# Performance work log

Measured on AMD Instinct MI355X. Metric: run time of the kernel, lower is better.

## Reference

```python
import jax, jax.numpy as jnp
import numpy as np

B, L, D, N_HEADS = 4, 8192, 1024, 16
HD = D // N_HEADS
MASK_NEG = -1e10


def setup_inputs() -> dict:
    key = jax.random.key(0)
    ks = jax.random.split(key, 5)
    # xavier_normal std for square Dense: sqrt(2/(fan_in+fan_out))
    std = (2.0 / (D + D)) ** 0.5
    return {
        "query": jax.random.normal(ks[0], (B, L, D), dtype=jnp.float32),
        "mask": jax.random.bernoulli(ks[1], 0.1, (B, L)),  # True = masked out
        "Wq": std * jax.random.normal(ks[2], (D, D), dtype=jnp.float32),
        "bq": jnp.zeros((D,), dtype=jnp.float32),
        "Wk": std * jax.random.normal(ks[3], (D, D), dtype=jnp.float32),
        "bk": jnp.zeros((D,), dtype=jnp.float32),
        "Wv": std * jax.random.normal(ks[4], (D, D), dtype=jnp.float32),
        "bv": jnp.zeros((D,), dtype=jnp.float32),
    }


def reference(query, mask, Wq, bq, Wk, bk, Wv, bv):
    # Self-attention: key = value = query (original falls back when key/value are None)
    q = query @ Wq + bq  # [B, L, D]
    k = query @ Wk + bk
    v = query @ Wv + bv
    # split heads: b l (n h) -> b l n h
    qs = q.reshape(B, L, N_HEADS, HD)
    ks_ = k.reshape(B, L, N_HEADS, HD)
    vs = v.reshape(B, L, N_HEADS, HD)
    m = mask[:, :, None, None]  # [B, L, 1, 1], broadcast over heads & dims
    K = jnp.where(m, MASK_NEG, ks_)
    V = jnp.where(m, 0.0, vs)
    # elu kernel feature map: phi(x) = elu(x) + 1 (elu(-1e10)+1 -> 0 for masked keys)
    phiK = jax.nn.elu(K) + 1.0
    phiQ = jax.nn.elu(qs) + 1.0
    # per-head kv summary: [B, N, HD_k, HD_v]
    kv = jnp.einsum('blnk,blnv->bnkv', phiK, V)
    # FAITHFUL to original einsum 'blk,bkv->blk': sums kv over v, elementwise with phiQ
    kv_sum = kv.sum(-1)  # [B, N, HD]
    out = phiQ * kv_sum[:, None, :, :]  # [B, L, N, HD]
    # combine heads: b l n h -> b l (n h)
    return out.reshape(B, L, D)
```

## Files before the change

### kernel.cpp

```cpp
#include <hip/hip_runtime.h>

typedef unsigned short u16;
typedef unsigned int u32;
typedef __attribute__((ext_vector_type(8))) short s16x8;
typedef __attribute__((ext_vector_type(4))) float f32x4;

#define GAS __attribute__((address_space(1)))
#define LAS __attribute__((address_space(3)))

#define BB 4
#define LL 8192
#define DD 1024
#define NH 16
#define HD 64
#define MROWS (BB * LL)
#define NWBT 2064

__device__ __forceinline__ u16 f2bf(float f) {
  u32 u = __builtin_bit_cast(u32, f);
  u32 r = (u + 0x7FFFu + ((u >> 16) & 1u)) >> 16;
  return (u16)r;
}
__device__ __forceinline__ float bf2f(u32 lo) {
  return __builtin_bit_cast(float, lo << 16);
}

__device__ __forceinline__ void async16(const void* g, void* l) {
  __builtin_amdgcn_global_load_lds((const GAS u32*)g, (LAS u32*)l, 16, 0, 0);
}

__device__ __forceinline__ bool get_mask(const void* mp, int row, int mode) {
  if (mode == 2) return ((const unsigned char*)mp)[row] != 0;
  if (mode == 1) return ((const float*)mp)[row] != 0.f;
  return ((const int*)mp)[row] != 0;
}

__global__ void build_wbt(const float* __restrict__ Wq, const float* __restrict__ Wk,
                          u16* __restrict__ WbT) {
  __shared__ float t[32][33];
  const int n0 = blockIdx.x * 32;
  const int k0 = blockIdx.y * 32;
  const float* W = (n0 >> 10) == 0 ? Wq : Wk;
  const int nloc = n0 & 1023;
  const int tx = threadIdx.x, ty = threadIdx.y;
#pragma unroll
  for (int j = 0; j < 32; j += 8)
    t[ty + j][tx] = W[(size_t)(k0 + ty + j) * DD + nloc + tx];
  __syncthreads();
#pragma unroll
  for (int j = 0; j < 32; j += 8)
    WbT[(size_t)(n0 + ty + j) * DD + k0 + tx] = f2bf(t[tx][ty + j]);
}

__global__ void build_aux(const float* __restrict__ Wv, const float* __restrict__ bq,
                          const float* __restrict__ bk, const float* __restrict__ bv,
                          const u32* __restrict__ m,
                          u16* __restrict__ WbT, float* __restrict__ bcat,
                          int* __restrict__ flag) {
  const int blk = blockIdx.x;
  const int tid = threadIdx.x;
  if (blk < 64) {
    int i = blk * 256 + tid;
    int k = i >> 4, h = i & 15;
    float s = 0.f;
    const float* p = Wv + (size_t)k * DD + h * HD;
#pragma unroll 8
    for (int j = 0; j < 64; ++j) s += p[j];
    WbT[(size_t)(2048 + h) * DD + k] = f2bf(s);
  } else if (blk < 73) {
    int i = (blk - 64) * 256 + tid;
    if (i < 1024) bcat[i] = bq[i];
    else if (i < 2048) bcat[i] = bk[i - 1024];
    else if (i < 2064) {
      float s = 0.f;
      const float* p = bv + (i - 2048) * HD;
#pragma unroll 8
      for (int j = 0; j < 64; ++j) s += p[j];
      bcat[i] = s;
    }
  } else {
    int i = (blk - 73) * 256 + tid;
    u32 v = m[i];
    int f = 0;
    if (v == 0x3F800000u) f = 1;
    else if (v > 1u) f = 2;
    if (f) atomicMax(flag, f);
  }
}

__global__ __launch_bounds__(256) void prep_q(
    const float* __restrict__ query, const u16* __restrict__ WbT,
    const float* __restrict__ bcat, const void* __restrict__ maskp,
    const int* __restrict__ mmode,
    u16* __restrict__ qb, float* __restrict__ sV) {
  __shared__ float sVp[2][16][16];
  const int tid = threadIdx.x;
  const int lane = tid & 63;
  const int w = tid >> 6;
  const int wl = w >> 1;
  const int ks = w & 1;
  const int l15 = lane & 15, l16 = lane >> 4;
  const int row0 = blockIdx.x * 32 + wl * 16;
  const int arow = row0 + l15;

  const float* qrow = query + (size_t)arow * DD + ks * 512 + l16 * 8;
  u16* qbrow = qb + (size_t)arow * DD + ks * 512 + l16 * 8;
  const u16* wrow = WbT + (size_t)(2048 + l15) * DD + ks * 512 + l16 * 8;

  f32x4 acc = {};
#pragma unroll
  for (int mac = 0; mac < 2; ++mac) {
    float4 qv[16];
    s16x8 wv[8];
#pragma unroll
    for (int s = 0; s < 8; ++s) {
      const int off = mac * 256 + s * 32;
      qv[s * 2] = *(const float4*)(qrow + off);
      qv[s * 2 + 1] = *(const float4*)(qrow + off + 4);
      wv[s] = *(const s16x8*)(wrow + off);
    }
#pragma unroll
    for (int s = 0; s < 8; ++s) {
      s16x8 o;
      o[0] = (short)f2bf(qv[s * 2].x);     o[1] = (short)f2bf(qv[s * 2].y);
      o[2] = (short)f2bf(qv[s * 2].z);     o[3] = (short)f2bf(qv[s * 2].w);
      o[4] = (short)f2bf(qv[s * 2 + 1].x); o[5] = (short)f2bf(qv[s * 2 + 1].y);
      o[6] = (short)f2bf(qv[s * 2 + 1].z); o[7] = (short)f2bf(qv[s * 2 + 1].w);
      *(s16x8*)(qbrow + mac * 256 + s * 32) = o;
      acc = __builtin_amdgcn_mfma_f32_16x16x32_bf16(o, wv[s], acc, 0, 0, 0);
    }
  }

  if (ks == 1) {
#pragma unroll
    for (int r = 0; r < 4; ++r) sVp[wl][l16 * 4 + r][l15] = acc[r];
  }
  __syncthreads();
  if (ks == 0) {
    const int mode = *mmode;
#pragma unroll
    for (int r = 0; r < 4; ++r) {
      const int row = row0 + l16 * 4 + r;
      const bool msk = get_mask(maskp, row, mode);
      float v = acc[r] + sVp[wl][l16 * 4 + r][l15] + bcat[2048 + l15];
      sV[(size_t)row * NH + l15] = msk ? 0.f : v;
    }
  }
}

#define AOFF(buf) ((buf) * 12288)
#define BOFF(buf) ((buf) * 12288 + 4096)

__global__ __launch_bounds__(512, 4) void gemm_qkv(
    const u16* __restrict__ qb, const u16* __restrict__ WbT,
    const float* __restrict__ bcat, const void* __restrict__ maskp,
    const int* __restrict__ mmode,
    const float* __restrict__ sV, float* __restrict__ kv,
    float* __restrict__ out, int phase) {
  __shared__ __align__(16) u16 lds[24576];
  const int tid = threadIdx.x;
  const int lane = tid & 63;
  const int w = tid >> 6;
  const int wm = w & 1, wn = w >> 1;
  const int l15 = lane & 15, l16 = lane >> 4;

  const int bid = blockIdx.x;
  const int swz = (bid & 7) * 128 + (bid >> 3);
  const int mt = swz >> 2;
  const int nt = swz & 3;
  const int row0 = mt * 128;
  const int col0 = (phase ? 1024 : 0) + nt * 256;

  f32x4 acc[4][4] = {};

#define STAGE_A(buf, kt) do {                                               \
    int row_ = tid >> 2, slot_ = tid & 3;                                   \
    int c_ = slot_ ^ ((row_ >> 1) & 3);                                     \
    async16(qb + (size_t)(row0 + row_) * DD + (kt) * 32 + c_ * 8,           \
            lds + AOFF(buf) + tid * 8);                                     \
  } while (0)

#define STAGE_B(buf, kt) do {                                               \
    _Pragma("unroll")                                                       \
    for (int j_ = 0; j_ < 2; ++j_) {                                        \
      int li_ = tid + j_ * 512;                                             \
      int row_ = li_ >> 2, slot_ = li_ & 3;                                 \
      int c_ = slot_ ^ ((row_ >> 1) & 3);                                   \
      async16(WbT + (size_t)(col0 + row_) * DD + (kt) * 32 + c_ * 8,        \
              lds + BOFF(buf) + li_ * 8);                                   \
    }                                                                       \
  } while (0)

#define LDA(buf, a) do {                                                    \
    _Pragma("unroll")                                                       \
    for (int mi_ = 0; mi_ < 4; ++mi_) {                                     \
      int r_ = wm * 64 + mi_ * 16 + l15;                                    \
      a[mi_] = *(const s16x8*)(lds + AOFF(buf) + r_ * 32 +                  \
                               ((l16 ^ ((r_ >> 1) & 3)) * 8));              \
    }                                                                       \
  } while (0)

#define LDB2(buf, nb, b) do {                                               \
    _Pragma("unroll")                                                       \
    for (int q_ = 0; q_ < 2; ++q_) {                                        \
      int r_ = wn * 64 + ((nb)*2 + q_) * 16 + l15;                          \
      b[q_] = *(const s16x8*)(lds + BOFF(buf) + r_ * 32 +                   \
                              ((l16 ^ ((r_ >> 1) & 3)) * 8));               \
    }                                                                       \
  } while (0)

#define MM(a, b, nb) do {                                                   \
    __builtin_amdgcn_s_setprio(1);                                          \
    _Pragma("unroll")                                                       \
    for (int mi_ = 0; mi_ < 4; ++mi_) {                                     \
      acc[mi_][(nb)*2] = __builtin_amdgcn_mfma_f32_16x16x32_bf16(           \
          a[mi_], b[0], acc[mi_][(nb)*2], 0, 0, 0);                         \
      acc[mi_][(nb)*2 + 1] = __builtin_amdgcn_mfma_f32_16x16x32_bf16(       \
          a[mi_], b[1], acc[mi_][(nb)*2 + 1], 0, 0, 0);                     \
    }                                                                       \
    __builtin_amdgcn_s_setprio(0);                                          \
  } while (0)

#define BAR() __builtin_amdgcn_s_barrier()
#define VMW1() asm volatile("s_waitcnt vmcnt(1)" ::: "memory")
#define VMW3() asm volatile("s_waitcnt vmcnt(3)" ::: "memory")
#define VMW0() asm volatile("s_waitcnt vmcnt(0)" ::: "memory")

  STAGE_A(0, 0); STAGE_B(0, 0); STAGE_A(1, 1); STAGE_B(1, 1);
  VMW3();
  BAR();

  for (int t = 0; t < 30; t += 2) {
    s16x8 a[4], b[2];
    LDA(0, a); LDB2(0, 0, b);
    if (t > 0) STAGE_B(1, t + 1);
    BAR(); MM(a, b, 0); BAR();
    LDB2(0, 1, b);
    STAGE_A(0, t + 2);
    BAR(); MM(a, b, 1); VMW1(); BAR();
    LDA(1, a); LDB2(1, 0, b);
    STAGE_B(0, t + 2);
    BAR(); MM(a, b, 0); BAR();
    LDB2(1, 1, b);
    STAGE_A(1, t + 3);
    BAR(); MM(a, b, 1); VMW1(); BAR();
  }

  {
    s16x8 a[4], b[2];
    LDA(0, a); LDB2(0, 0, b);
    STAGE_B(1, 31);
    BAR(); MM(a, b, 0); BAR();
    LDB2(0, 1, b);
    BAR(); MM(a, b, 1); VMW0(); BAR();
    LDA(1, a); LDB2(1, 0, b);
    BAR(); MM(a, b, 0); BAR();
    LDB2(1, 1, b);
    BAR(); MM(a, b, 1);
  }

  const int mode = *mmode;
  const int lanec = lane & 15, laneq = lane >> 4;
  const int wcol0 = col0 + wn * 64;
  const int b_ = row0 >> 13;

  if (phase == 1) {
    const int n = (wcol0 - 1024) >> 6;
    float pc[4] = {0.f, 0.f, 0.f, 0.f};
#pragma unroll
    for (int mi = 0; mi < 4; ++mi) {
#pragma unroll
      for (int r = 0; r < 4; ++r) {
        const int row = row0 + wm * 64 + mi * 16 + laneq * 4 + r;
        const bool msk = get_mask(maskp, row, mode);
        if (!msk) {
          const float sv = sV[(size_t)row * NH + n];
#pragma unroll
          for (int ni = 0; ni < 4; ++ni) {
            const int col = wcol0 + ni * 16 + lanec;
            float v = acc[mi][ni][r] + bcat[col];
            float phi = v > 0.f ? v + 1.f : __expf(v);
            pc[ni] += phi * sv;
          }
        }
      }
    }
#pragma unroll
    for (int ni = 0; ni < 4; ++ni) {
      pc[ni] += __shfl_xor(pc[ni], 16);
      pc[ni] += __shfl_xor(pc[ni], 32);
    }
    if (laneq == 0) {
#pragma unroll
      for (int ni = 0; ni < 4; ++ni) {
        const int colk = wcol0 - 1024 + ni * 16 + lanec;
        atomicAdd(&kv[b_ * DD + colk], pc[ni]);
      }
    }
  } else {
    float kvv[4];
#pragma unroll
    for (int ni = 0; ni < 4; ++ni)
      kvv[ni] = kv[b_ * DD + wcol0 + ni * 16 + lanec];
#pragma unroll
    for (int mi = 0; mi < 4; ++mi) {
#pragma unroll
      for (int r = 0; r < 4; ++r) {
        const int row = row0 + wm * 64 + mi * 16 + laneq * 4 + r;
#pragma unroll
        for (int ni = 0; ni < 4; ++ni) {
          const int col = wcol0 + ni * 16 + lanec;
          float v = acc[mi][ni][r] + bcat[col];
          float phi = v > 0.f ? v + 1.f : __expf(v);
          out[(size_t)row * DD + col] = phi * kvv[ni];
        }
      }
    }
  }
}

extern "C" void kernel_launch(void* const* d_in, const int* in_sizes, int n_in,
                              void* d_out, int out_size, void* d_ws, size_t ws_size,
                              hipStream_t stream) {
  const float* query = (const float*)d_in[0];
  const void* maskp = d_in[1];
  const float* Wq = (const float*)d_in[2];
  const float* bq = (const float*)d_in[3];
  const float* Wk = (const float*)d_in[4];
  const float* bk = (const float*)d_in[5];
  const float* Wv = (const float*)d_in[6];
  const float* bv = (const float*)d_in[7];
  float* out = (float*)d_out;

  char* ws = (char*)d_ws;
  u16* qb = (u16*)ws;            ws += (size_t)MROWS * DD * 2;
  u16* WbT = (u16*)ws;           ws += (size_t)NWBT * DD * 2;
  float* sV = (float*)ws;        ws += (size_t)MROWS * NH * 4;
  float* bcat = (float*)ws;      ws += (size_t)NWBT * 4;
  float* kv = (float*)ws;        ws += (size_t)BB * DD * 4;
  int* mflag = (int*)ws;         ws += 256;

  hipMemsetAsync(kv, 0, (size_t)BB * DD * 4 + 256, stream);

  build_wbt<<<dim3(2048 / 32, DD / 32), dim3(32, 8), 0, stream>>>(Wq, Wk, WbT);
  build_aux<<<105, 256, 0, stream>>>(Wv, bq, bk, bv, (const u32*)maskp, WbT, bcat, mflag);
  prep_q<<<MROWS / 32, 256, 0, stream>>>(query, WbT, bcat, maskp, mflag, qb, sV);
  gemm_qkv<<<1024, 512, 0, stream>>>(qb, WbT, bcat, maskp, mflag, sV, kv, out, 1);
  gemm_qkv<<<1024, 512, 0, stream>>>(qb, WbT, bcat, maskp, mflag, sV, kv, out, 0);
}
```

Baseline: 410.5 us.

## Widen GEMM block tile to 128x512 for more A-tile reuse

The GEMM tile per block grows from 128x256 to 128x512: each wave now computes 64x128 with 32 accumulators, B staging doubles, LDS grows to 80KB, and the grid halves to 512 blocks. The epilogue now covers two heads per wave, reading two sV values. The aim is to halve A-tile reloads and raise MFMA work per LDS read. In exchange register pressure roughly doubles, occupancy drops (launch bounds 2), and 512 blocks may leave fewer waves per CU to hide latency on a 256-CU device.

```diff
diff --git a/kernel.cpp b/kernel.cpp
--- a/kernel.cpp
+++ b/kernel.cpp
@@ -148,16 +148,16 @@
   }
 }
 
-#define AOFF(buf) ((buf) * 12288)
-#define BOFF(buf) ((buf) * 12288 + 4096)
-
-__global__ __launch_bounds__(512, 4) void gemm_qkv(
+#define AOFF(buf) ((buf) * 4096)
+#define BOFF(buf) (8192 + (buf) * 16384)
+
+__global__ __launch_bounds__(512, 2) void gemm_qkv(
     const u16* __restrict__ qb, const u16* __restrict__ WbT,
     const float* __restrict__ bcat, const void* __restrict__ maskp,
     const int* __restrict__ mmode,
     const float* __restrict__ sV, float* __restrict__ kv,
     float* __restrict__ out, int phase) {
-  __shared__ __align__(16) u16 lds[24576];
+  __shared__ __align__(16) u16 lds[40960];
   const int tid = threadIdx.x;
   const int lane = tid & 63;
   const int w = tid >> 6;
@@ -165,13 +165,13 @@
   const int l15 = lane & 15, l16 = lane >> 4;
 
   const int bid = blockIdx.x;
-  const int swz = (bid & 7) * 128 + (bid >> 3);
-  const int mt = swz >> 2;
-  const int nt = swz & 3;
+  const int swz = (bid & 7) * 64 + (bid >> 3);
+  const int mt = swz >> 1;
+  const int nt = swz & 1;
   const int row0 = mt * 128;
-  const int col0 = (phase ? 1024 : 0) + nt * 256;
-
-  f32x4 acc[4][4] = {};
+  const int col0 = (phase ? 1024 : 0) + nt * 512;
+
+  f32x4 acc[4][8] = {};
 
 #define STAGE_A(buf, kt) do {                                               \
     int row_ = tid >> 2, slot_ = tid & 3;                                   \
@@ -182,7 +182,7 @@
 
 #define STAGE_B(buf, kt) do {                                               \
     _Pragma("unroll")                                                       \
-    for (int j_ = 0; j_ < 2; ++j_) {                                        \
+    for (int j_ = 0; j_ < 4; ++j_) {                                        \
       int li_ = tid + j_ * 512;                                             \
       int row_ = li_ >> 2, slot_ = li_ & 3;                                 \
       int c_ = slot_ ^ ((row_ >> 1) & 3);                                   \
@@ -200,10 +200,10 @@
     }                                                                       \
   } while (0)
 
-#define LDB2(buf, nb, b) do {                                               \
+#define LDB4(buf, nb, b) do {                                               \
     _Pragma("unroll")                                                       \
-    for (int q_ = 0; q_ < 2; ++q_) {                                        \
-      int r_ = wn * 64 + ((nb)*2 + q_) * 16 + l15;                          \
+    for (int q_ = 0; q_ < 4; ++q_) {                                        \
+      int r_ = wn * 128 + (nb) * 64 + q_ * 16 + l15;                        \
       b[q_] = *(const s16x8*)(lds + BOFF(buf) + r_ * 32 +                   \
                               ((l16 ^ ((r_ >> 1) & 3)) * 8));               \
     }                                                                       \
@@ -213,60 +213,61 @@
     __builtin_amdgcn_s_setprio(1);                                          \
     _Pragma("unroll")                                                       \
     for (int mi_ = 0; mi_ < 4; ++mi_) {                                     \
-      acc[mi_][(nb)*2] = __builtin_amdgcn_mfma_f32_16x16x32_bf16(           \
-          a[mi_], b[0], acc[mi_][(nb)*2], 0, 0, 0);                         \
-      acc[mi_][(nb)*2 + 1] = __builtin_amdgcn_mfma_f32_16x16x32_bf16(       \
-          a[mi_], b[1], acc[mi_][(nb)*2 + 1], 0, 0, 0);                     \
+      _Pragma("unroll")                                                     \
+      for (int q_ = 0; q_ < 4; ++q_) {                                      \
+        acc[mi_][(nb)*4 + q_] = __builtin_amdgcn_mfma_f32_16x16x32_bf16(    \
+            a[mi_], b[q_], acc[mi_][(nb)*4 + q_], 0, 0, 0);                 \
+      }                                                                     \
     }                                                                       \
     __builtin_amdgcn_s_setprio(0);                                          \
   } while (0)
 
 #define BAR() __builtin_amdgcn_s_barrier()
 #define VMW1() asm volatile("s_waitcnt vmcnt(1)" ::: "memory")
-#define VMW3() asm volatile("s_waitcnt vmcnt(3)" ::: "memory")
+#define VMW5() asm volatile("s_waitcnt vmcnt(5)" ::: "memory")
 #define VMW0() asm volatile("s_waitcnt vmcnt(0)" ::: "memory")
 
   STAGE_A(0, 0); STAGE_B(0, 0); STAGE_A(1, 1); STAGE_B(1, 1);
-  VMW3();
+  VMW5();
   BAR();
 
   for (int t = 0; t < 30; t += 2) {
-    s16x8 a[4], b[2];
-    LDA(0, a); LDB2(0, 0, b);
+    s16x8 a[4], b[4];
+    LDA(0, a); LDB4(0, 0, b);
     if (t > 0) STAGE_B(1, t + 1);
     BAR(); MM(a, b, 0); BAR();
-    LDB2(0, 1, b);
+    LDB4(0, 1, b);
     STAGE_A(0, t + 2);
     BAR(); MM(a, b, 1); VMW1(); BAR();
-    LDA(1, a); LDB2(1, 0, b);
+    LDA(1, a); LDB4(1, 0, b);
     STAGE_B(0, t + 2);
     BAR(); MM(a, b, 0); BAR();
-    LDB2(1, 1, b);
+    LDB4(1, 1, b);
     STAGE_A(1, t + 3);
     BAR(); MM(a, b, 1); VMW1(); BAR();
   }
 
   {
-    s16x8 a[4], b[2];
-    LDA(0, a); LDB2(0, 0, b);
+    s16x8 a[4], b[4];
+    LDA(0, a); LDB4(0, 0, b);
     STAGE_B(1, 31);
     BAR(); MM(a, b, 0); BAR();
-    LDB2(0, 1, b);
+    LDB4(0, 1, b);
     BAR(); MM(a, b, 1); VMW0(); BAR();
-    LDA(1, a); LDB2(1, 0, b);
+    LDA(1, a); LDB4(1, 0, b);
     BAR(); MM(a, b, 0); BAR();
-    LDB2(1, 1, b);
+    LDB4(1, 1, b);
     BAR(); MM(a, b, 1);
   }
 
   const int mode = *mmode;
   const int lanec = lane & 15, laneq = lane >> 4;
-  const int wcol0 = col0 + wn * 64;
+  const int wcol0 = col0 + wn * 128;
   const int b_ = row0 >> 13;
 
   if (phase == 1) {
-    const int n = (wcol0 - 1024) >> 6;
-    float pc[4] = {0.f, 0.f, 0.f, 0.f};
+    const int h0 = (wcol0 - 1024) >> 6;
+    float pc[8] = {0.f, 0.f, 0.f, 0.f, 0.f, 0.f, 0.f, 0.f};
 #pragma unroll
     for (int mi = 0; mi < 4; ++mi) {
 #pragma unroll
@@ -274,45 +275,46 @@
         const int row = row0 + wm * 64 + mi * 16 + laneq * 4 + r;
         const bool msk = get_mask(maskp, row, mode);
         if (!msk) {
-          const float sv = sV[(size_t)row * NH + n];
-#pragma unroll
-          for (int ni = 0; ni < 4; ++ni) {
-            const int col = wcol0 + ni * 16 + lanec;
-            float v = acc[mi][ni][r] + bcat[col];
+          const float sv0 = sV[(size_t)row * NH + h0];
+          const float sv1 = sV[(size_t)row * NH + h0 + 1];
+#pragma unroll
+          for (int nj = 0; nj < 8; ++nj) {
+            const int col = wcol0 + nj * 16 + lanec;
+            float v = acc[mi][nj][r] + bcat[col];
             float phi = v > 0.f ? v + 1.f : __expf(v);
-            pc[ni] += phi * sv;
+            pc[nj] += phi * (nj < 4 ? sv0 : sv1);
           }
         }
       }
     }
 #pragma unroll
-    for (int ni = 0; ni < 4; ++ni) {
-      pc[ni] += __shfl_xor(pc[ni], 16);
-      pc[ni] += __shfl_xor(pc[ni], 32);
+    for (int nj = 0; nj < 8; ++nj) {
+      pc[nj] += __shfl_xor(pc[nj], 16);
+      pc[nj] += __shfl_xor(pc[nj], 32);
     }
     if (laneq == 0) {
 #pragma unroll
-      for (int ni = 0; ni < 4; ++ni) {
-        const int colk = wcol0 - 1024 + ni * 16 + lanec;
-        atomicAdd(&kv[b_ * DD + colk], pc[ni]);
+      for (int nj = 0; nj < 8; ++nj) {
+        const int colk = wcol0 - 1024 + nj * 16 + lanec;
+        atomicAdd(&kv[b_ * DD + colk], pc[nj]);
       }
     }
   } else {
-    float kvv[4];
-#pragma unroll
-    for (int ni = 0; ni < 4; ++ni)
-      kvv[ni] = kv[b_ * DD + wcol0 + ni * 16 + lanec];
+    float kvv[8];
+#pragma unroll
+    for (int nj = 0; nj < 8; ++nj)
+      kvv[nj] = kv[b_ * DD + wcol0 + nj * 16 + lanec];
 #pragma unroll
     for (int mi = 0; mi < 4; ++mi) {
 #pragma unroll
       for (int r = 0; r < 4; ++r) {
         const int row = row0 + wm * 64 + mi * 16 + laneq * 4 + r;
 #pragma unroll
-        for (int ni = 0; ni < 4; ++ni) {
-          const int col = wcol0 + ni * 16 + lanec;
-          float v = acc[mi][ni][r] + bcat[col];
+        for (int nj = 0; nj < 8; ++nj) {
+          const int col = wcol0 + nj * 16 + lanec;
+          float v = acc[mi][nj][r] + bcat[col];
           float phi = v > 0.f ? v + 1.f : __expf(v);
-          out[(size_t)row * DD + col] = phi * kvv[ni];
+          out[(size_t)row * DD + col] = phi * kvv[nj];
         }
       }
     }
@@ -345,6 +347,6 @@
   build_wbt<<<dim3(2048 / 32, DD / 32), dim3(32, 8), 0, stream>>>(Wq, Wk, WbT);
   build_aux<<<105, 256, 0, stream>>>(Wv, bq, bk, bv, (const u32*)maskp, WbT, bcat, mflag);
   prep_q<<<MROWS / 32, 256, 0, stream>>>(query, WbT, bcat, maskp, mflag, qb, sV);
-  gemm_qkv<<<1024, 512, 0, stream>>>(qb, WbT, bcat, maskp, mflag, sV, kv, out, 1);
-  gemm_qkv<<<1024, 512, 0, stream>>>(qb, WbT, bcat, maskp, mflag, sV, kv, out, 0);
-}
+  gemm_qkv<<<512, 512, 0, stream>>>(qb, WbT, bcat, maskp, mflag, sV, kv, out, 1);
+  gemm_qkv<<<512, 512, 0, stream>>>(qb, WbT, bcat, maskp, mflag, sV, kv, out, 0);
+}
```

Result: no change. 416.7 us (+1.5%).

## Deepen QKV GEMM K-loop pipeline to four LDS stages with register prefetch

Applied to the files above, without the earlier changes.

Replaces the two-buffer LDS staging in the QKV projection GEMM with a four-slot ring buffer, where A and B tiles are issued three k-steps ahead. Fragments for the next MFMA group are read from LDS into separate registers while the current group computes, and each phase now needs one barrier instead of two. LDS use doubles and launch bounds drop from 4 to 2 blocks per CU. This trades occupancy for deeper latency hiding within each block.

```diff
diff --git a/kernel.cpp b/kernel.cpp
--- a/kernel.cpp
+++ b/kernel.cpp
@@ -148,16 +148,16 @@
   }
 }
 
-#define AOFF(buf) ((buf) * 12288)
-#define BOFF(buf) ((buf) * 12288 + 4096)
-
-__global__ __launch_bounds__(512, 4) void gemm_qkv(
+#define AOFF(u) ((u) * 4096)
+#define BOFF(u) (16384 + (u) * 8192)
+
+__global__ __launch_bounds__(512, 2) void gemm_qkv(
     const u16* __restrict__ qb, const u16* __restrict__ WbT,
     const float* __restrict__ bcat, const void* __restrict__ maskp,
     const int* __restrict__ mmode,
     const float* __restrict__ sV, float* __restrict__ kv,
     float* __restrict__ out, int phase) {
-  __shared__ __align__(16) u16 lds[24576];
+  __shared__ __align__(16) u16 lds[49152];
   const int tid = threadIdx.x;
   const int lane = tid & 63;
   const int w = tid >> 6;
@@ -173,38 +173,38 @@
 
   f32x4 acc[4][4] = {};
 
-#define STAGE_A(buf, kt) do {                                               \
+#define STAGE_A(u, kt) do {                                                 \
     int row_ = tid >> 2, slot_ = tid & 3;                                   \
     int c_ = slot_ ^ ((row_ >> 1) & 3);                                     \
     async16(qb + (size_t)(row0 + row_) * DD + (kt) * 32 + c_ * 8,           \
-            lds + AOFF(buf) + tid * 8);                                     \
-  } while (0)
-
-#define STAGE_B(buf, kt) do {                                               \
+            lds + AOFF(u) + tid * 8);                                       \
+  } while (0)
+
+#define STAGE_B(u, kt) do {                                                 \
     _Pragma("unroll")                                                       \
     for (int j_ = 0; j_ < 2; ++j_) {                                        \
       int li_ = tid + j_ * 512;                                             \
       int row_ = li_ >> 2, slot_ = li_ & 3;                                 \
       int c_ = slot_ ^ ((row_ >> 1) & 3);                                   \
       async16(WbT + (size_t)(col0 + row_) * DD + (kt) * 32 + c_ * 8,        \
-              lds + BOFF(buf) + li_ * 8);                                   \
+              lds + BOFF(u) + li_ * 8);                                     \
     }                                                                       \
   } while (0)
 
-#define LDA(buf, a) do {                                                    \
+#define LDA(u, a) do {                                                      \
     _Pragma("unroll")                                                       \
     for (int mi_ = 0; mi_ < 4; ++mi_) {                                     \
       int r_ = wm * 64 + mi_ * 16 + l15;                                    \
-      a[mi_] = *(const s16x8*)(lds + AOFF(buf) + r_ * 32 +                  \
+      a[mi_] = *(const s16x8*)(lds + AOFF(u) + r_ * 32 +                    \
                                ((l16 ^ ((r_ >> 1) & 3)) * 8));              \
     }                                                                       \
   } while (0)
 
-#define LDB2(buf, nb, b) do {                                               \
+#define LDB2(u, nb, b) do {                                                 \
     _Pragma("unroll")                                                       \
     for (int q_ = 0; q_ < 2; ++q_) {                                        \
       int r_ = wn * 64 + ((nb)*2 + q_) * 16 + l15;                          \
-      b[q_] = *(const s16x8*)(lds + BOFF(buf) + r_ * 32 +                   \
+      b[q_] = *(const s16x8*)(lds + BOFF(u) + r_ * 32 +                     \
                               ((l16 ^ ((r_ >> 1) & 3)) * 8));               \
     }                                                                       \
   } while (0)
@@ -222,41 +222,83 @@
   } while (0)
 
 #define BAR() __builtin_amdgcn_s_barrier()
-#define VMW1() asm volatile("s_waitcnt vmcnt(1)" ::: "memory")
-#define VMW3() asm volatile("s_waitcnt vmcnt(3)" ::: "memory")
-#define VMW0() asm volatile("s_waitcnt vmcnt(0)" ::: "memory")
-
-  STAGE_A(0, 0); STAGE_B(0, 0); STAGE_A(1, 1); STAGE_B(1, 1);
-  VMW3();
-  BAR();
-
-  for (int t = 0; t < 30; t += 2) {
-    s16x8 a[4], b[2];
-    LDA(0, a); LDB2(0, 0, b);
-    if (t > 0) STAGE_B(1, t + 1);
-    BAR(); MM(a, b, 0); BAR();
-    LDB2(0, 1, b);
-    STAGE_A(0, t + 2);
-    BAR(); MM(a, b, 1); VMW1(); BAR();
-    LDA(1, a); LDB2(1, 0, b);
-    STAGE_B(0, t + 2);
-    BAR(); MM(a, b, 0); BAR();
-    LDB2(1, 1, b);
-    STAGE_A(1, t + 3);
-    BAR(); MM(a, b, 1); VMW1(); BAR();
+#define VMW(n) asm volatile("s_waitcnt vmcnt(" #n ")" ::: "memory")
+
+  s16x8 aE[4], aO[4], bc[2], bn[2];
+
+  STAGE_A(0, 0); STAGE_B(0, 0);
+  STAGE_A(1, 1); STAGE_B(1, 1);
+  STAGE_A(2, 2); STAGE_B(2, 2);
+  VMW(6); BAR();
+  LDA(0, aE); LDB2(0, 0, bc);
+
+  for (int T = 0; T < 28; T += 4) {
+    STAGE_A(3, T + 3);
+    LDB2(0, 1, bn);
+    MM(aE, bc, 0);
+    VMW(4); BAR();
+    STAGE_B(3, T + 3);
+    LDA(1, aO); LDB2(1, 0, bc);
+    MM(aE, bn, 1);
+    VMW(6); BAR();
+    STAGE_A(0, T + 4);
+    LDB2(1, 1, bn);
+    MM(aO, bc, 0);
+    VMW(4); BAR();
+    STAGE_B(0, T + 4);
+    LDA(2, aE); LDB2(2, 0, bc);
+    MM(aO, bn, 1);
+    VMW(6); BAR();
+    STAGE_A(1, T + 5);
+    LDB2(2, 1, bn);
+    MM(aE, bc, 0);
+    VMW(4); BAR();
+    STAGE_B(1, T + 5);
+    LDA(3, aO); LDB2(3, 0, bc);
+    MM(aE, bn, 1);
+    VMW(6); BAR();
+    STAGE_A(2, T + 6);
+    LDB2(3, 1, bn);
+    MM(aO, bc, 0);
+    VMW(4); BAR();
+    STAGE_B(2, T + 6);
+    LDA(0, aE); LDB2(0, 0, bc);
+    MM(aO, bn, 1);
+    VMW(6); BAR();
   }
 
   {
-    s16x8 a[4], b[2];
-    LDA(0, a); LDB2(0, 0, b);
-    STAGE_B(1, 31);
-    BAR(); MM(a, b, 0); BAR();
-    LDB2(0, 1, b);
-    BAR(); MM(a, b, 1); VMW0(); BAR();
-    LDA(1, a); LDB2(1, 0, b);
-    BAR(); MM(a, b, 0); BAR();
-    LDB2(1, 1, b);
-    BAR(); MM(a, b, 1);
+    STAGE_A(3, 31);
+    LDB2(0, 1, bn);
+    MM(aE, bc, 0);
+    VMW(4); BAR();
+
+    STAGE_B(3, 31);
+    LDA(1, aO); LDB2(1, 0, bc);
+    MM(aE, bn, 1);
+    VMW(6); BAR();
+
+    LDB2(1, 1, bn);
+    MM(aO, bc, 0);
+    VMW(3); BAR();
+
+    LDA(2, aE); LDB2(2, 0, bc);
+    MM(aO, bn, 1);
+    VMW(3); BAR();
+
+    LDB2(2, 1, bn);
+    MM(aE, bc, 0);
+    VMW(0); BAR();
+
+    LDA(3, aO); LDB2(3, 0, bc);
+    MM(aE, bn, 1);
+    BAR();
+
+    LDB2(3, 1, bn);
+    MM(aO, bc, 0);
+    BAR();
+
+    MM(aO, bn, 1);
   }
 
   const int mode = *mmode;
```

Result: slower. 424.6 us (+3.4%).
